# Optimization experiments

Measured on AMD Instinct MI355X. Metric: run time of the kernel, lower is better.

## Reference

```python
import jax, jax.numpy as jnp
import numpy as np

N, D_IN, Z, K = 65536, 512, 128, 1024


def setup_inputs() -> dict:
    key = jax.random.key(0)
    k1, k2, k3 = jax.random.split(key, 3)
    x = jax.random.normal(k1, (N, D_IN), dtype=jnp.float32)
    # Dense(z_units) params (glorot-ish scale)
    W = jax.random.normal(k2, (D_IN, Z), dtype=jnp.float32) * (1.0 / np.sqrt(D_IN))
    b = jnp.zeros((Z,), dtype=jnp.float32)
    # VQ codebook [k_discrete, z_units]
    codebook = jax.random.normal(k3, (K, Z), dtype=jnp.float32)
    return {"x": x, "W": W, "b": b, "codebook": codebook}


def reference(x, W, b, codebook):
    # z_embed: Dense projection to z_units
    z_continuous = x @ W + b  # [N, Z]
    # Euclidean distances to codebook entries, computed via the expanded
    # quadratic form (avoids materializing the [N, K, Z] broadcast tensor).
    sq = (jnp.sum(z_continuous * z_continuous, axis=-1, keepdims=True)
          - 2.0 * (z_continuous @ codebook.T)
          + jnp.sum(codebook * codebook, axis=-1))  # [N, K]
    distances = jnp.sqrt(jnp.maximum(sq, 0.0))
    k_nearest = jnp.argmin(distances, axis=-1)  # [N] int
    z_quantised = codebook[k_nearest]  # gather -> [N, Z]
    z_one_hot = jax.nn.one_hot(k_nearest, K, dtype=z_continuous.dtype)  # [N, K]
    # straight-through estimator
    z_straight_through = z_continuous + jax.lax.stop_gradient(z_quantised - z_continuous)
    # perplexity stats (stored as a layer attribute in the original; computed here
    # for faithfulness but not returned, matching call()'s return signature)
    avg_probs = jnp.mean(z_one_hot, axis=0)
    _perplexity = jnp.exp(-jnp.sum(avg_probs * jnp.log(avg_probs + 1e-10)))
    return (z_straight_through, z_quantised, z_continuous, z_one_hot)
```

## Files before the change

kernel.cpp:

```cpp
#include <hip/hip_runtime.h>
#include <cstddef>

#define NROWS 65536
#define DIN   512
#define ZDIM  128
#define KCB   1024

typedef float  f32x4  __attribute__((ext_vector_type(4)));
typedef short  short8 __attribute__((ext_vector_type(8)));
typedef __bf16 bf16x8 __attribute__((ext_vector_type(8)));
typedef unsigned short ushort_t;
typedef unsigned int   uint_t;

#define CB_CHB 24576
#define CB_SPB 8192
#define W_CHB  24576
#define W_SPB  8192
#define CNORM_OFF 786432
#define WF_OFF    790528
#define WS_NEEDED (790528 + 393216)

__device__ inline ushort_t bf_rtn(float v) {
  uint_t u = __float_as_uint(v);
  uint_t r = (u + 0x7fffu + ((u >> 16) & 1u)) >> 16;
  return (ushort_t)r;
}
__device__ inline float bf_up(ushort_t b) { return __uint_as_float(((uint_t)b) << 16); }
__device__ inline bf16x8 as_bf(short8 s) {
  union { short8 s; bf16x8 b; } u; u.s = s; return u.b;
}
__device__ inline void split3(float v, ushort_t& s1, ushort_t& s2, ushort_t& s3) {
  s1 = bf_rtn(v);  float f1 = bf_up(s1);
  float r1 = v - f1; s2 = bf_rtn(r1); float f2 = bf_up(s2);
  float r2 = r1 - f2; s3 = bf_rtn(r2);
}

__global__ __launch_bounds__(128) void ksplit2(
    const float* __restrict__ cbk, char* __restrict__ wsb)
{
  const int n = blockIdx.x, k = threadIdx.x;
  float v = cbk[(size_t)n * ZDIM + k];
  ushort_t s1, s2, s3; split3(v, s1, s2, s3);

  const int chunk = n >> 5, ct = (n >> 4) & 1;
  const int km = k & 31, ks = k >> 5;
  const int g = (km >> 2) & 3, h = (km >> 4) & 1, j = (km & 3) + 4 * h;
  const int l = 16 * g + (n & 15);
  char* base = wsb + chunk * CB_CHB + ct * 4096 + ks * 1024 + l * 16 + j * 2;
  *(ushort_t*)(base + 0 * CB_SPB) = s1;
  *(ushort_t*)(base + 1 * CB_SPB) = s2;
  *(ushort_t*)(base + 2 * CB_SPB) = s3;

  float c2 = v * v;
#pragma unroll
  for (int m = 1; m < 64; m <<= 1) c2 += __shfl_xor(c2, m);
  __shared__ float wsum[2];
  if ((threadIdx.x & 63) == 0) wsum[threadIdx.x >> 6] = c2;
  __syncthreads();
  if (threadIdx.x == 0)
    *(float*)(wsb + CNORM_OFF + (size_t)n * 4) = wsum[0] + wsum[1];
}

__global__ __launch_bounds__(256) void wsplit(
    const float* __restrict__ W, char* __restrict__ wsb)
{
  const int idx = blockIdx.x * 256 + threadIdx.x;
  const int k = idx >> 7, col = idx & 127;
  float v = W[(size_t)k * ZDIM + col];
  ushort_t s1, s2, s3; split3(v, s1, s2, s3);

  const int kc = k >> 5, km = k & 31;
  const int g = (km >> 2) & 3, h = (km >> 4) & 1, j = (km & 3) + 4 * h;
  const int ct = col >> 4, l = 16 * g + (col & 15);
  char* base = wsb + WF_OFF + kc * W_CHB + ct * 1024 + l * 16 + j * 2;
  *(ushort_t*)(base + 0 * W_SPB) = s1;
  *(ushort_t*)(base + 1 * W_SPB) = s2;
  *(ushort_t*)(base + 2 * W_SPB) = s3;
}

__global__ __launch_bounds__(256, 2) void k1_mfma(
    const float* __restrict__ x, const char* __restrict__ wfs,
    const float* __restrict__ b, float* __restrict__ z)
{
  __shared__ __align__(16) char wbuf[2 * W_CHB];

  const int t = threadIdx.x, w = t >> 6, l = t & 63;
  const int g = l >> 4, c16 = l & 15;
  const int bm = blockIdx.x;

  f32x4 acc[2][8];
#pragma unroll
  for (int rt = 0; rt < 2; ++rt)
#pragma unroll
    for (int ct = 0; ct < 8; ++ct) acc[rt][ct] = (f32x4){0.f, 0.f, 0.f, 0.f};

  const size_t rowb[2] = {
    ((size_t)bm * 128 + w * 32 + 0 * 16 + c16) * DIN,
    ((size_t)bm * 128 + w * 32 + 1 * 16 + c16) * DIN };

  f32x4 wreg[6];
#pragma unroll
  for (int it = 0; it < 6; ++it)
    wreg[it] = *(const f32x4*)(wfs + it * 4096 + t * 16);
  f32x4 xcur[2][2];
#pragma unroll
  for (int rt = 0; rt < 2; ++rt)
#pragma unroll
    for (int h = 0; h < 2; ++h)
      xcur[rt][h] = *(const f32x4*)(x + rowb[rt] + 4 * g + 16 * h);
#pragma unroll
  for (int it = 0; it < 6; ++it)
    *(f32x4*)(wbuf + it * 4096 + t * 16) = wreg[it];
  __syncthreads();

  for (int kc = 0; kc < 16; ++kc) {
    const char* buf = wbuf + (size_t)(kc & 1) * W_CHB;
    const bool more = (kc + 1) < 16;
    f32x4 xnext[2][2];
    if (more) {
#pragma unroll
      for (int it = 0; it < 6; ++it)
        wreg[it] = *(const f32x4*)(wfs + (size_t)(kc + 1) * W_CHB + it * 4096 + t * 16);
#pragma unroll
      for (int rt = 0; rt < 2; ++rt)
#pragma unroll
        for (int h = 0; h < 2; ++h)
          xnext[rt][h] = *(const f32x4*)(x + rowb[rt] + (kc + 1) * 32 + 4 * g + 16 * h);
    }

    short8 a1[2], a2[2], a3[2];
#pragma unroll
    for (int rt = 0; rt < 2; ++rt)
#pragma unroll
      for (int h = 0; h < 2; ++h)
#pragma unroll
        for (int j = 0; j < 4; ++j) {
          ushort_t q1, q2, q3; split3(xcur[rt][h][j], q1, q2, q3);
          a1[rt][4 * h + j] = (short)q1;
          a2[rt][4 * h + j] = (short)q2;
          a3[rt][4 * h + j] = (short)q3;
        }

#pragma unroll
    for (int ct = 0; ct < 8; ++ct) {
      const char* bp = buf + ct * 1024 + l * 16;
      short8 b1 = *(const short8*)(bp + 0 * W_SPB);
      short8 b2 = *(const short8*)(bp + 1 * W_SPB);
      short8 b3 = *(const short8*)(bp + 2 * W_SPB);
#pragma unroll
      for (int rt = 0; rt < 2; ++rt) {
        f32x4 a = acc[rt][ct];
        a = __builtin_amdgcn_mfma_f32_16x16x32_bf16(as_bf(a1[rt]), as_bf(b1), a, 0, 0, 0);
        a = __builtin_amdgcn_mfma_f32_16x16x32_bf16(as_bf(a1[rt]), as_bf(b2), a, 0, 0, 0);
        a = __builtin_amdgcn_mfma_f32_16x16x32_bf16(as_bf(a2[rt]), as_bf(b1), a, 0, 0, 0);
        a = __builtin_amdgcn_mfma_f32_16x16x32_bf16(as_bf(a1[rt]), as_bf(b3), a, 0, 0, 0);
        a = __builtin_amdgcn_mfma_f32_16x16x32_bf16(as_bf(a2[rt]), as_bf(b2), a, 0, 0, 0);
        a = __builtin_amdgcn_mfma_f32_16x16x32_bf16(as_bf(a3[rt]), as_bf(b1), a, 0, 0, 0);
        acc[rt][ct] = a;
      }
    }

    if (more) {
      char* nbuf = wbuf + (size_t)((kc + 1) & 1) * W_CHB;
#pragma unroll
      for (int it = 0; it < 6; ++it)
        *(f32x4*)(nbuf + it * 4096 + t * 16) = wreg[it];
#pragma unroll
      for (int rt = 0; rt < 2; ++rt)
#pragma unroll
        for (int h = 0; h < 2; ++h) xcur[rt][h] = xnext[rt][h];
    }
    __syncthreads();
  }

#pragma unroll
  for (int ct = 0; ct < 8; ++ct) {
    float bb = b[ct * 16 + c16];
#pragma unroll
    for (int rt = 0; rt < 2; ++rt)
#pragma unroll
      for (int i = 0; i < 4; ++i) {
        size_t row = (size_t)bm * 128 + w * 32 + rt * 16 + 4 * g + i;
        z[row * ZDIM + ct * 16 + c16] = acc[rt][ct][i] + bb;
      }
  }
}

__global__ __launch_bounds__(256, 2) void k2_mfma2(
    const float* __restrict__ zc, const float* __restrict__ cbk,
    const char* __restrict__ cbs, const float* __restrict__ cnorm,
    float* __restrict__ zst, float* __restrict__ zq, float* __restrict__ oh)
{
  __shared__ __align__(16) char buf2[2 * CB_CHB];
  __shared__ int karr[128];

  const int t = threadIdx.x, w = t >> 6, l = t & 63;
  const int g = l >> 4, c16 = l & 15;
  const int bm = blockIdx.x;

  f32x4 streg[6];
#pragma unroll
  for (int it = 0; it < 6; ++it)
    streg[it] = *(const f32x4*)(cbs + it * 4096 + t * 16);

  short8 a1[2][4], a2[2][4], a3[2][4];
  float anorm[2][4];
#pragma unroll
  for (int rt = 0; rt < 2; ++rt) {
    const size_t rb = ((size_t)bm * 128 + w * 32 + rt * 16 + c16) * ZDIM;
    float psum = 0.f;
#pragma unroll
    for (int ks = 0; ks < 4; ++ks)
#pragma unroll
      for (int h = 0; h < 2; ++h) {
        f32x4 v = *(const f32x4*)(zc + rb + ks * 32 + 4 * g + 16 * h);
#pragma unroll
        for (int j = 0; j < 4; ++j) {
          ushort_t q1, q2, q3; split3(v[j], q1, q2, q3);
          a1[rt][ks][4 * h + j] = (short)q1;
          a2[rt][ks][4 * h + j] = (short)q2;
          a3[rt][ks][4 * h + j] = (short)q3;
          psum += v[j] * v[j];
        }
      }
    psum += __shfl_xor(psum, 16);
    psum += __shfl_xor(psum, 32);
#pragma unroll
    for (int i = 0; i < 4; ++i) anorm[rt][i] = __shfl(psum, 4 * g + i);
  }

#pragma unroll
  for (int it = 0; it < 6; ++it)
    *(f32x4*)(buf2 + it * 4096 + t * 16) = streg[it];
  __syncthreads();

  float fmin[2][4]; int kmin[2][4];
#pragma unroll
  for (int rt = 0; rt < 2; ++rt)
#pragma unroll
    for (int i = 0; i < 4; ++i) { fmin[rt][i] = 3.402823466e38f; kmin[rt][i] = 0; }

  for (int c = 0; c < 32; ++c) {
    const char* buf = buf2 + (size_t)(c & 1) * CB_CHB;
    const bool more = (c + 1) < 32;
    if (more) {
#pragma unroll
      for (int it = 0; it < 6; ++it)
        streg[it] = *(const f32x4*)(cbs + (size_t)(c + 1) * CB_CHB + it * 4096 + t * 16);
    }

    {
      const size_t orow = (size_t)(bm * 128 + c * 4 + (t >> 6)) * KCB;
#pragma unroll
      for (int u = 0; u < 4; ++u) {
        f32x4 zv = {0.f, 0.f, 0.f, 0.f};
        *(f32x4*)(oh + orow + (t & 63) * 4 + u * 256) = zv;
      }
    }

    float cn0 = cnorm[c * 32 + c16];
    float cn1 = cnorm[c * 32 + 16 + c16];

#pragma unroll
    for (int ct = 0; ct < 2; ++ct) {
      f32x4 pa[2];
#pragma unroll
      for (int rt = 0; rt < 2; ++rt) pa[rt] = (f32x4){0.f, 0.f, 0.f, 0.f};
#pragma unroll
      for (int ks = 0; ks < 4; ++ks) {
        const char* bp = buf + ct * 4096 + ks * 1024 + l * 16;
        short8 b1 = *(const short8*)(bp + 0 * CB_SPB);
        short8 b2 = *(const short8*)(bp + 1 * CB_SPB);
        short8 b3 = *(const short8*)(bp + 2 * CB_SPB);
#pragma unroll
        for (int rt = 0; rt < 2; ++rt) {
          f32x4 a = pa[rt];
          a = __builtin_amdgcn_mfma_f32_16x16x32_bf16(as_bf(a1[rt][ks]), as_bf(b1), a, 0, 0, 0);
          a = __builtin_amdgcn_mfma_f32_16x16x32_bf16(as_bf(a1[rt][ks]), as_bf(b2), a, 0, 0, 0);
          a = __builtin_amdgcn_mfma_f32_16x16x32_bf16(as_bf(a2[rt][ks]), as_bf(b1), a, 0, 0, 0);
          a = __builtin_amdgcn_mfma_f32_16x16x32_bf16(as_bf(a1[rt][ks]), as_bf(b3), a, 0, 0, 0);
          a = __builtin_amdgcn_mfma_f32_16x16x32_bf16(as_bf(a2[rt][ks]), as_bf(b2), a, 0, 0, 0);
          a = __builtin_amdgcn_mfma_f32_16x16x32_bf16(as_bf(a3[rt][ks]), as_bf(b1), a, 0, 0, 0);
          pa[rt] = a;
        }
      }
      const int colb = c * 32 + ct * 16 + c16;
      const float cn = ct ? cn1 : cn0;
#pragma unroll
      for (int rt = 0; rt < 2; ++rt)
#pragma unroll
        for (int i = 0; i < 4; ++i) {
          float f = (anorm[rt][i] - 2.f * pa[rt][i]) + cn;
          if (f < fmin[rt][i]) { fmin[rt][i] = f; kmin[rt][i] = colb; }
        }
    }

    if (more) {
      char* nbuf = buf2 + (size_t)((c + 1) & 1) * CB_CHB;
#pragma unroll
      for (int it = 0; it < 6; ++it)
        *(f32x4*)(nbuf + it * 4096 + t * 16) = streg[it];
    }
    __syncthreads();
  }

#pragma unroll
  for (int m = 1; m < 16; m <<= 1) {
#pragma unroll
    for (int rt = 0; rt < 2; ++rt)
#pragma unroll
      for (int i = 0; i < 4; ++i) {
        float f2 = __shfl_xor(fmin[rt][i], m);
        int   k2 = __shfl_xor(kmin[rt][i], m);
        if (f2 < fmin[rt][i] || (f2 == fmin[rt][i] && k2 < kmin[rt][i])) {
          fmin[rt][i] = f2; kmin[rt][i] = k2;
        }
      }
  }
  if (c16 == 0) {
#pragma unroll
    for (int rt = 0; rt < 2; ++rt)
#pragma unroll
      for (int i = 0; i < 4; ++i)
        karr[w * 32 + rt * 16 + 4 * g + i] = kmin[rt][i];
  }
  __syncthreads();

  for (int it = 0; it < 64; ++it) {
    int r = it * 2 + (t >> 7);
    int col = t & 127;
    size_t row = (size_t)bm * 128 + r;
    float v = cbk[(size_t)karr[r] * ZDIM + col];
    zst[row * ZDIM + col] = v;
    zq[row * ZDIM + col] = v;
  }

  if (t < 128) {
    oh[(size_t)(bm * 128 + t) * KCB + karr[t]] = 1.0f;
  }
}

__global__ __launch_bounds__(256) void k1_gemm(
    const float* __restrict__ x, const float* __restrict__ W,
    const float* __restrict__ b, float* __restrict__ z)
{
  __shared__ float xs[32][68];
  __shared__ float ws[32][132];

  const int t  = threadIdx.x;
  const int tx = t & 15, ty = t >> 4;
  const int bm = blockIdx.x;

  float acc[4][8];
#pragma unroll
  for (int i = 0; i < 4; ++i)
#pragma unroll
    for (int j = 0; j < 8; ++j) acc[i][j] = 0.f;

  const int sr  = t >> 2;
  const int skb = (t & 3) * 8;
  const int wkk = t >> 3;
  const int wcol = (t & 7) * 16;

  for (int k0 = 0; k0 < DIN; k0 += 32) {
    float4 v0 = *reinterpret_cast<const float4*>(&x[(size_t)(bm * 64 + sr) * DIN + k0 + skb]);
    float4 v1 = *reinterpret_cast<const float4*>(&x[(size_t)(bm * 64 + sr) * DIN + k0 + skb + 4]);
    xs[skb + 0][sr] = v0.x; xs[skb + 1][sr] = v0.y; xs[skb + 2][sr] = v0.z; xs[skb + 3][sr] = v0.w;
    xs[skb + 4][sr] = v1.x; xs[skb + 5][sr] = v1.y; xs[skb + 6][sr] = v1.z; xs[skb + 7][sr] = v1.w;
#pragma unroll
    for (int u = 0; u < 4; ++u) {
      float4 wv = *reinterpret_cast<const float4*>(&W[(size_t)(k0 + wkk) * ZDIM + wcol + u * 4]);
      *reinterpret_cast<float4*>(&ws[wkk][wcol + u * 4]) = wv;
    }
    __syncthreads();
#pragma unroll
    for (int kk = 0; kk < 32; ++kk) {
      float4 xv = *reinterpret_cast<float4*>(&xs[kk][ty * 4]);
      float4 wa = *reinterpret_cast<float4*>(&ws[kk][tx * 4]);
      float4 wb = *reinterpret_cast<float4*>(&ws[kk][64 + tx * 4]);
      float xr[4] = {xv.x, xv.y, xv.z, xv.w};
      float wr[8] = {wa.x, wa.y, wa.z, wa.w, wb.x, wb.y, wb.z, wb.w};
#pragma unroll
      for (int i = 0; i < 4; ++i)
#pragma unroll
        for (int j = 0; j < 8; ++j) acc[i][j] += xr[i] * wr[j];
    }
    __syncthreads();
  }

  float4 ba = *reinterpret_cast<const float4*>(&b[tx * 4]);
  float4 bb = *reinterpret_cast<const float4*>(&b[64 + tx * 4]);
#pragma unroll
  for (int i = 0; i < 4; ++i) {
    size_t row = (size_t)bm * 64 + ty * 4 + i;
    float4 oa = {acc[i][0] + ba.x, acc[i][1] + ba.y, acc[i][2] + ba.z, acc[i][3] + ba.w};
    float4 ob = {acc[i][4] + bb.x, acc[i][5] + bb.y, acc[i][6] + bb.z, acc[i][7] + bb.w};
    *reinterpret_cast<float4*>(&z[row * ZDIM + tx * 4]) = oa;
    *reinterpret_cast<float4*>(&z[row * ZDIM + 64 + tx * 4]) = ob;
  }
}

__global__ __launch_bounds__(256) void k2_vq(
    const float* __restrict__ zc, const float* __restrict__ cbk,
    float* __restrict__ zst, float* __restrict__ zq, float* __restrict__ oh)
{
  __shared__ float zt[128][68];
  __shared__ float ct[32][132];
  __shared__ float pc[128][2];
  __shared__ float csqc[128];
  __shared__ float Ap[64][4];
  __shared__ float Al[64];
  __shared__ float fbuf[64][17];
  __shared__ int   ibuf[64][17];
  __shared__ int   karr[64];

  const int t  = threadIdx.x;
  const int tx = t & 15, ty = t >> 4;
  const int bm = blockIdx.x;

  {
    const int r = t >> 2, kb = (t & 3) * 32;
    float asum = 0.f;
#pragma unroll
    for (int u = 0; u < 8; ++u) {
      float4 v = *reinterpret_cast<const float4*>(&zc[(size_t)(bm * 64 + r) * ZDIM + kb + u * 4]);
      zt[kb + u * 4 + 0][r] = v.x; zt[kb + u * 4 + 1][r] = v.y;
      zt[kb + u * 4 + 2][r] = v.z; zt[kb + u * 4 + 3][r] = v.w;
      asum += v.x * v.x + v.y * v.y + v.z * v.z + v.w * v.w;
    }
    Ap[r][t & 3] = asum;
  }
  __syncthreads();
  if (t < 64) Al[t] = (Ap[t][0] + Ap[t][1]) + (Ap[t][2] + Ap[t][3]);

  float fmin[4];
  int   kmin[4];
#pragma unroll
  for (int i = 0; i < 4; ++i) { fmin[i] = 3.4e38f; kmin[i] = 0; }

  const int scol = t >> 1, skb = (t & 1) * 16;

  for (int chunk = 0; chunk < 8; ++chunk) {
    float acc[4][8];
#pragma unroll
    for (int i = 0; i < 4; ++i)
#pragma unroll
      for (int j = 0; j < 8; ++j) acc[i][j] = 0.f;
    float cpart = 0.f;

    for (int ks = 0; ks < 4; ++ks) {
      __syncthreads();
#pragma unroll
      for (int u = 0; u < 4; ++u) {
        float4 v = *reinterpret_cast<const float4*>(
            &cbk[(size_t)(chunk * 128 + scol) * ZDIM + ks * 32 + skb + u * 4]);
        ct[skb + u * 4 + 0][scol] = v.x; ct[skb + u * 4 + 1][scol] = v.y;
        ct[skb + u * 4 + 2][scol] = v.z; ct[skb + u * 4 + 3][scol] = v.w;
        cpart += v.x * v.x + v.y * v.y + v.z * v.z + v.w * v.w;
      }
      __syncthreads();
#pragma unroll
      for (int kk = 0; kk < 32; ++kk) {
        float4 xv = *reinterpret_cast<float4*>(&zt[ks * 32 + kk][ty * 4]);
        float4 wa = *reinterpret_cast<float4*>(&ct[kk][tx * 4]);
        float4 wb = *reinterpret_cast<float4*>(&ct[kk][64 + tx * 4]);
        float xr[4] = {xv.x, xv.y, xv.z, xv.w};
        float wr[8] = {wa.x, wa.y, wa.z, wa.w, wb.x, wb.y, wb.z, wb.w};
#pragma unroll
        for (int i = 0; i < 4; ++i)
#pragma unroll
          for (int j = 0; j < 8; ++j) acc[i][j] += xr[i] * wr[j];
      }
    }

    pc[scol][t & 1] = cpart;
    __syncthreads();
    if (t < 128) csqc[t] = pc[t][0] + pc[t][1];
    __syncthreads();

#pragma unroll
    for (int i = 0; i < 4; ++i) {
      float Ar = Al[ty * 4 + i];
#pragma unroll
      for (int j = 0; j < 8; ++j) {
        int colL = (j < 4) ? (tx * 4 + j) : (64 + tx * 4 + (j - 4));
        float B = 2.f * acc[i][j];
        float f = (Ar - B) + csqc[colL];
        int col = chunk * 128 + colL;
        if (f < fmin[i] || (f == fmin[i] && col < kmin[i])) { fmin[i] = f; kmin[i] = col; }
      }
    }
  }

#pragma unroll
  for (int i = 0; i < 4; ++i) { fbuf[ty * 4 + i][tx] = fmin[i]; ibuf[ty * 4 + i][tx] = kmin[i]; }
  __syncthreads();
  if (t < 64) {
    float bf = fbuf[t][0]; int bi = ibuf[t][0];
    for (int e = 1; e < 16; ++e) {
      float f2 = fbuf[t][e]; int i2 = ibuf[t][e];
      if (f2 < bf || (f2 == bf && i2 < bi)) { bf = f2; bi = i2; }
    }
    karr[t] = bi;
  }
  __syncthreads();

  for (int it = 0; it < 32; ++it) {
    int r = it * 2 + (t >> 7);
    int col = t & 127;
    size_t row = (size_t)bm * 64 + r;
    float v = cbk[(size_t)karr[r] * ZDIM + col];
    zst[row * ZDIM + col] = v;
    zq[row * ZDIM + col] = v;
  }

  for (int r = 0; r < 64; ++r) {
    int k = karr[r];
    float4 v = {0.f, 0.f, 0.f, 0.f};
    if ((k >> 2) == t) {
      float* vv = reinterpret_cast<float*>(&v);
      vv[k & 3] = 1.f;
    }
    *reinterpret_cast<float4*>(&oh[(size_t)(bm * 64 + r) * KCB + t * 4]) = v;
  }
}

extern "C" void kernel_launch(void* const* d_in, const int* in_sizes, int n_in,
                              void* d_out, int out_size, void* d_ws, size_t ws_size,
                              hipStream_t stream) {
  const float* x   = (const float*)d_in[0];
  const float* W   = (const float*)d_in[1];
  const float* b   = (const float*)d_in[2];
  const float* cbk = (const float*)d_in[3];

  float* out = (float*)d_out;
  float* zst = out;
  float* zq  = out + (size_t)NROWS * ZDIM;
  float* zc  = out + (size_t)2 * NROWS * ZDIM;
  float* oh  = out + (size_t)3 * NROWS * ZDIM;

  if (ws_size >= (size_t)WS_NEEDED) {
    char* wsb = (char*)d_ws;
    ksplit2<<<KCB, 128, 0, stream>>>(cbk, wsb);
    wsplit<<<256, 256, 0, stream>>>(W, wsb);
    k1_mfma<<<NROWS / 128, 256, 0, stream>>>(x, wsb + WF_OFF, b, zc);
    k2_mfma2<<<NROWS / 128, 256, 0, stream>>>(
        zc, cbk, wsb, (const float*)(wsb + CNORM_OFF), zst, zq, oh);
  } else {
    k1_gemm<<<NROWS / 64, 256, 0, stream>>>(x, W, b, zc);
    k2_vq<<<NROWS / 64, 256, 0, stream>>>(zc, cbk, zst, zq, oh);
  }
}
```

Before: 169.0 us.

## Fuse projection GEMM and VQ distance kernel, staging z tile in LDS

Merges the projection kernel and the codebook-distance kernel into one launch. Each block keeps its 128x128 z tile in a swizzled shared-memory buffer, so the VQ stage no longer reads z back from global memory. The kernel also prefetches codebook norms one chunk ahead, uses nontemporal stores for the zc, one-hot, zq and zst outputs, and vectorises the gather of codebook rows. In exchange, shared memory per block grows to 64KB plus karr, which may limit occupancy to fewer blocks per CU than the launch bound of 2 requests.

```diff
diff --git a/kernel.cpp b/kernel.cpp
--- a/kernel.cpp
+++ b/kernel.cpp
@@ -19,6 +19,8 @@
 #define CNORM_OFF 786432
 #define WF_OFF    790528
 #define WS_NEEDED (790528 + 393216)
+
+#define ZWORD(r, c) ((r) * 128 + ((c) ^ (((r) & 7) << 2)))
 
 __device__ inline ushort_t bf_rtn(float v) {
   uint_t u = __float_as_uint(v);
@@ -78,11 +80,16 @@
   *(ushort_t*)(base + 2 * W_SPB) = s3;
 }
 
-__global__ __launch_bounds__(256, 2) void k1_mfma(
+__global__ __launch_bounds__(256, 2) void fused(
     const float* __restrict__ x, const char* __restrict__ wfs,
-    const float* __restrict__ b, float* __restrict__ z)
+    const float* __restrict__ b, const char* __restrict__ cbs,
+    const float* __restrict__ cnorm, const float* __restrict__ cbk,
+    float* __restrict__ zst, float* __restrict__ zq,
+    float* __restrict__ zc, float* __restrict__ oh)
 {
-  __shared__ __align__(16) char wbuf[2 * W_CHB];
+  __shared__ __align__(16) char smem[65536];
+  __shared__ int karr[128];
+  float* zw = (float*)smem;
 
   const int t = threadIdx.x, w = t >> 6, l = t & 63;
   const int g = l >> 4, c16 = l & 15;
@@ -110,11 +117,11 @@
       xcur[rt][h] = *(const f32x4*)(x + rowb[rt] + 4 * g + 16 * h);
 #pragma unroll
   for (int it = 0; it < 6; ++it)
-    *(f32x4*)(wbuf + it * 4096 + t * 16) = wreg[it];
+    *(f32x4*)(smem + it * 4096 + t * 16) = wreg[it];
   __syncthreads();
 
   for (int kc = 0; kc < 16; ++kc) {
-    const char* buf = wbuf + (size_t)(kc & 1) * W_CHB;
+    const char* buf = smem + (size_t)(kc & 1) * W_CHB;
     const bool more = (kc + 1) < 16;
     f32x4 xnext[2][2];
     if (more) {
@@ -161,7 +168,7 @@
     }
 
     if (more) {
-      char* nbuf = wbuf + (size_t)((kc + 1) & 1) * W_CHB;
+      char* nbuf = smem + (size_t)((kc + 1) & 1) * W_CHB;
 #pragma unroll
       for (int it = 0; it < 6; ++it)
         *(f32x4*)(nbuf + it * 4096 + t * 16) = wreg[it];
@@ -176,50 +183,40 @@
 #pragma unroll
   for (int ct = 0; ct < 8; ++ct) {
     float bb = b[ct * 16 + c16];
+    const int col = ct * 16 + c16;
 #pragma unroll
     for (int rt = 0; rt < 2; ++rt)
 #pragma unroll
       for (int i = 0; i < 4; ++i) {
-        size_t row = (size_t)bm * 128 + w * 32 + rt * 16 + 4 * g + i;
-        z[row * ZDIM + ct * 16 + c16] = acc[rt][ct][i] + bb;
-      }
-  }
-}
-
-__global__ __launch_bounds__(256, 2) void k2_mfma2(
-    const float* __restrict__ zc, const float* __restrict__ cbk,
-    const char* __restrict__ cbs, const float* __restrict__ cnorm,
-    float* __restrict__ zst, float* __restrict__ zq, float* __restrict__ oh)
-{
-  __shared__ __align__(16) char buf2[2 * CB_CHB];
-  __shared__ int karr[128];
-
-  const int t = threadIdx.x, w = t >> 6, l = t & 63;
-  const int g = l >> 4, c16 = l & 15;
-  const int bm = blockIdx.x;
+        const int rl = w * 32 + rt * 16 + 4 * g + i;
+        zw[ZWORD(rl, col)] = acc[rt][ct][i] + bb;
+      }
+  }
+  __syncthreads();
 
   f32x4 streg[6];
 #pragma unroll
   for (int it = 0; it < 6; ++it)
     streg[it] = *(const f32x4*)(cbs + it * 4096 + t * 16);
 
-  short8 a1[2][4], a2[2][4], a3[2][4];
+  short8 a1f[2][4], a2f[2][4], a3f[2][4];
   float anorm[2][4];
 #pragma unroll
   for (int rt = 0; rt < 2; ++rt) {
-    const size_t rb = ((size_t)bm * 128 + w * 32 + rt * 16 + c16) * ZDIM;
+    const int rl = w * 32 + rt * 16 + c16;
     float psum = 0.f;
 #pragma unroll
     for (int ks = 0; ks < 4; ++ks)
 #pragma unroll
       for (int h = 0; h < 2; ++h) {
-        f32x4 v = *(const f32x4*)(zc + rb + ks * 32 + 4 * g + 16 * h);
+        const int c0 = ks * 32 + 4 * g + 16 * h;
+        f32x4 v = *(const f32x4*)&zw[ZWORD(rl, c0)];
 #pragma unroll
         for (int j = 0; j < 4; ++j) {
           ushort_t q1, q2, q3; split3(v[j], q1, q2, q3);
-          a1[rt][ks][4 * h + j] = (short)q1;
-          a2[rt][ks][4 * h + j] = (short)q2;
-          a3[rt][ks][4 * h + j] = (short)q3;
+          a1f[rt][ks][4 * h + j] = (short)q1;
+          a2f[rt][ks][4 * h + j] = (short)q2;
+          a3f[rt][ks][4 * h + j] = (short)q3;
           psum += v[j] * v[j];
         }
       }
@@ -229,9 +226,20 @@
     for (int i = 0; i < 4; ++i) anorm[rt][i] = __shfl(psum, 4 * g + i);
   }
 
+  {
+    const int r = t >> 1, half = (t & 1) * 64;
+    float* dst = zc + ((size_t)bm * 128 + r) * ZDIM;
+#pragma unroll
+    for (int u = 0; u < 16; ++u) {
+      const int c0 = half + u * 4;
+      f32x4 v = *(const f32x4*)&zw[ZWORD(r, c0)];
+      __builtin_nontemporal_store(v, (f32x4*)(dst + c0));
+    }
+  }
+  __syncthreads();
 #pragma unroll
   for (int it = 0; it < 6; ++it)
-    *(f32x4*)(buf2 + it * 4096 + t * 16) = streg[it];
+    *(f32x4*)(smem + it * 4096 + t * 16) = streg[it];
   __syncthreads();
 
   float fmin[2][4]; int kmin[2][4];
@@ -240,26 +248,27 @@
 #pragma unroll
     for (int i = 0; i < 4; ++i) { fmin[rt][i] = 3.402823466e38f; kmin[rt][i] = 0; }
 
+  float cn0 = cnorm[c16], cn1 = cnorm[16 + c16];
+
   for (int c = 0; c < 32; ++c) {
-    const char* buf = buf2 + (size_t)(c & 1) * CB_CHB;
+    const char* buf = smem + (size_t)(c & 1) * CB_CHB;
     const bool more = (c + 1) < 32;
+    float cn0n = 0.f, cn1n = 0.f;
     if (more) {
 #pragma unroll
       for (int it = 0; it < 6; ++it)
         streg[it] = *(const f32x4*)(cbs + (size_t)(c + 1) * CB_CHB + it * 4096 + t * 16);
+      cn0n = cnorm[(c + 1) * 32 + c16];
+      cn1n = cnorm[(c + 1) * 32 + 16 + c16];
     }
 
     {
-      const size_t orow = (size_t)(bm * 128 + c * 4 + (t >> 6)) * KCB;
-#pragma unroll
-      for (int u = 0; u < 4; ++u) {
-        f32x4 zv = {0.f, 0.f, 0.f, 0.f};
-        *(f32x4*)(oh + orow + (t & 63) * 4 + u * 256) = zv;
-      }
-    }
-
-    float cn0 = cnorm[c * 32 + c16];
-    float cn1 = cnorm[c * 32 + 16 + c16];
+      float* orow = oh + (size_t)(bm * 128 + c * 4 + (t >> 6)) * KCB + (t & 63) * 4;
+      const f32x4 zv = {0.f, 0.f, 0.f, 0.f};
+#pragma unroll
+      for (int u = 0; u < 4; ++u)
+        __builtin_nontemporal_store(zv, (f32x4*)(orow + u * 256));
+    }
 
 #pragma unroll
     for (int ct = 0; ct < 2; ++ct) {
@@ -275,12 +284,12 @@
 #pragma unroll
         for (int rt = 0; rt < 2; ++rt) {
           f32x4 a = pa[rt];
-          a = __builtin_amdgcn_mfma_f32_16x16x32_bf16(as_bf(a1[rt][ks]), as_bf(b1), a, 0, 0, 0);
-          a = __builtin_amdgcn_mfma_f32_16x16x32_bf16(as_bf(a1[rt][ks]), as_bf(b2), a, 0, 0, 0);
-          a = __builtin_amdgcn_mfma_f32_16x16x32_bf16(as_bf(a2[rt][ks]), as_bf(b1), a, 0, 0, 0);
-          a = __builtin_amdgcn_mfma_f32_16x16x32_bf16(as_bf(a1[rt][ks]), as_bf(b3), a, 0, 0, 0);
-          a = __builtin_amdgcn_mfma_f32_16x16x32_bf16(as_bf(a2[rt][ks]), as_bf(b2), a, 0, 0, 0);
-          a = __builtin_amdgcn_mfma_f32_16x16x32_bf16(as_bf(a3[rt][ks]), as_bf(b1), a, 0, 0, 0);
+          a = __builtin_amdgcn_mfma_f32_16x16x32_bf16(as_bf(a1f[rt][ks]), as_bf(b1), a, 0, 0, 0);
+          a = __builtin_amdgcn_mfma_f32_16x16x32_bf16(as_bf(a1f[rt][ks]), as_bf(b2), a, 0, 0, 0);
+          a = __builtin_amdgcn_mfma_f32_16x16x32_bf16(as_bf(a2f[rt][ks]), as_bf(b1), a, 0, 0, 0);
+          a = __builtin_amdgcn_mfma_f32_16x16x32_bf16(as_bf(a1f[rt][ks]), as_bf(b3), a, 0, 0, 0);
+          a = __builtin_amdgcn_mfma_f32_16x16x32_bf16(as_bf(a2f[rt][ks]), as_bf(b2), a, 0, 0, 0);
+          a = __builtin_amdgcn_mfma_f32_16x16x32_bf16(as_bf(a3f[rt][ks]), as_bf(b1), a, 0, 0, 0);
           pa[rt] = a;
         }
       }
@@ -296,10 +305,11 @@
     }
 
     if (more) {
-      char* nbuf = buf2 + (size_t)((c + 1) & 1) * CB_CHB;
+      char* nbuf = smem + (size_t)((c + 1) & 1) * CB_CHB;
 #pragma unroll
       for (int it = 0; it < 6; ++it)
         *(f32x4*)(nbuf + it * 4096 + t * 16) = streg[it];
+      cn0 = cn0n; cn1 = cn1n;
     }
     __syncthreads();
   }
@@ -326,13 +336,14 @@
   }
   __syncthreads();
 
-  for (int it = 0; it < 64; ++it) {
-    int r = it * 2 + (t >> 7);
-    int col = t & 127;
-    size_t row = (size_t)bm * 128 + r;
-    float v = cbk[(size_t)karr[r] * ZDIM + col];
-    zst[row * ZDIM + col] = v;
-    zq[row * ZDIM + col] = v;
+#pragma unroll
+  for (int it = 0; it < 16; ++it) {
+    const int idx = it * 256 + t;
+    const int r = idx >> 5, cq = (idx & 31) * 4;
+    f32x4 v = *(const f32x4*)&cbk[(size_t)karr[r] * ZDIM + cq];
+    const size_t off = ((size_t)bm * 128 + r) * ZDIM + cq;
+    __builtin_nontemporal_store(v, (f32x4*)(zst + off));
+    __builtin_nontemporal_store(v, (f32x4*)(zq + off));
   }
 
   if (t < 128) {
@@ -543,9 +554,9 @@
     char* wsb = (char*)d_ws;
     ksplit2<<<KCB, 128, 0, stream>>>(cbk, wsb);
     wsplit<<<256, 256, 0, stream>>>(W, wsb);
-    k1_mfma<<<NROWS / 128, 256, 0, stream>>>(x, wsb + WF_OFF, b, zc);
-    k2_mfma2<<<NROWS / 128, 256, 0, stream>>>(
-        zc, cbk, wsb, (const float*)(wsb + CNORM_OFF), zst, zq, oh);
+    fused<<<NROWS / 128, 256, 0, stream>>>(
+        x, wsb + WF_OFF, b, wsb, (const float*)(wsb + CNORM_OFF), cbk,
+        zst, zq, zc, oh);
   } else {
     k1_gemm<<<NROWS / 64, 256, 0, stream>>>(x, W, b, zc);
     k2_vq<<<NROWS / 64, 256, 0, stream>>>(zc, cbk, zst, zq, oh);
```

Result: slower. 212.9 us (+26.0%).

## Use single-bf16 distance pass with candidate threshold and exact fp32 refinement

Applied to the files above, without the earlier changes.

The distance GEMM now uses a single bf16 MFMA term instead of six split-precision products. It makes two passes: one to find an approximate per-row minimum, and one to collect codes within a margin of it, which are then rescored exactly in fp32 and reduced through atomic 64-bit keys. Zeroing the one-hot output moves into the projection kernel with nontemporal stores, and the gather writes become vectorized. Risks: the 0.25*sqrt(|z|^2) margin is a heuristic that might miss the true argmin, and the codebook is now streamed twice.

```diff
diff --git a/kernel.cpp b/kernel.cpp
--- a/kernel.cpp
+++ b/kernel.cpp
@@ -11,6 +11,7 @@
 typedef __bf16 bf16x8 __attribute__((ext_vector_type(8)));
 typedef unsigned short ushort_t;
 typedef unsigned int   uint_t;
+typedef unsigned long long u64_t;
 
 #define CB_CHB 24576
 #define CB_SPB 8192
@@ -33,6 +34,37 @@
   s1 = bf_rtn(v);  float f1 = bf_up(s1);
   float r1 = v - f1; s2 = bf_rtn(r1); float f2 = bf_up(s2);
   float r2 = r1 - f2; s3 = bf_rtn(r2);
+}
+
+__device__ inline void refine_one(uint_t packed, int bm, int w,
+    const float* __restrict__ zc, const float* __restrict__ cbk,
+    const float* __restrict__ cnorm, u64_t* rowkey)
+{
+  const int col = packed & 1023;
+  const int rowloc = (packed >> 10) & 31;
+  const int r = w * 32 + rowloc;
+  const float* zr = zc + ((size_t)bm * 128 + r) * ZDIM;
+  const float* cr = cbk + (size_t)col * ZDIM;
+  f32x4 dps = {0.f, 0.f, 0.f, 0.f}, aps = {0.f, 0.f, 0.f, 0.f};
+#pragma unroll
+  for (int u = 0; u < 32; ++u) {
+    f32x4 zv = *(const f32x4*)(zr + u * 4);
+    f32x4 cv = *(const f32x4*)(cr + u * 4);
+    dps += zv * cv;
+    aps += zv * zv;
+  }
+  float dot = (dps[0] + dps[1]) + (dps[2] + dps[3]);
+  float A   = (aps[0] + aps[1]) + (aps[2] + aps[3]);
+  float d = (A - 2.f * dot) + cnorm[col];
+  uint_t db = __float_as_uint(d);
+  db = (db & 0x80000000u) ? ~db : (db | 0x80000000u);
+  u64_t key = ((u64_t)db << 32) | (uint_t)col;
+  u64_t old = rowkey[r];
+  while (key < old) {
+    u64_t assumed = old;
+    old = atomicCAS(&rowkey[r], assumed, key);
+    if (old == assumed) break;
+  }
 }
 
 __global__ __launch_bounds__(128) void ksplit2(
@@ -78,9 +110,10 @@
   *(ushort_t*)(base + 2 * W_SPB) = s3;
 }
 
-__global__ __launch_bounds__(256, 2) void k1_mfma(
+__global__ __launch_bounds__(256, 2) void k1_oh(
     const float* __restrict__ x, const char* __restrict__ wfs,
-    const float* __restrict__ b, float* __restrict__ z)
+    const float* __restrict__ b, float* __restrict__ z,
+    float* __restrict__ oh)
 {
   __shared__ __align__(16) char wbuf[2 * W_CHB];
 
@@ -126,6 +159,14 @@
 #pragma unroll
         for (int h = 0; h < 2; ++h)
           xnext[rt][h] = *(const f32x4*)(x + rowb[rt] + (kc + 1) * 32 + 4 * g + 16 * h);
+    }
+
+    {
+      float* orow = oh + ((size_t)bm * 128 + kc * 8 + (t >> 5)) * KCB + (t & 31) * 4;
+      const f32x4 zv4 = {0.f, 0.f, 0.f, 0.f};
+#pragma unroll
+      for (int u = 0; u < 8; ++u)
+        __builtin_nontemporal_store(zv4, (f32x4*)(orow + u * 128));
     }
 
     short8 a1[2], a2[2], a3[2];
@@ -186,24 +227,25 @@
   }
 }
 
-__global__ __launch_bounds__(256, 2) void k2_mfma2(
+__global__ __launch_bounds__(256, 2) void k2f(
     const float* __restrict__ zc, const float* __restrict__ cbk,
     const char* __restrict__ cbs, const float* __restrict__ cnorm,
     float* __restrict__ zst, float* __restrict__ zq, float* __restrict__ oh)
 {
-  __shared__ __align__(16) char buf2[2 * CB_CHB];
+  __shared__ __align__(16) char sm[16384];
+  __shared__ u64_t rowkey[128];
+  __shared__ uint_t wpool[4][128];
+  __shared__ int wcnt[4];
   __shared__ int karr[128];
 
   const int t = threadIdx.x, w = t >> 6, l = t & 63;
   const int g = l >> 4, c16 = l & 15;
   const int bm = blockIdx.x;
 
-  f32x4 streg[6];
-#pragma unroll
-  for (int it = 0; it < 6; ++it)
-    streg[it] = *(const f32x4*)(cbs + it * 4096 + t * 16);
-
-  short8 a1[2][4], a2[2][4], a3[2][4];
+  if (t < 128) rowkey[t] = ~0ull;
+  if (t < 4) wcnt[t] = 0;
+
+  short8 a1f[2][4];
   float anorm[2][4];
 #pragma unroll
   for (int rt = 0; rt < 2; ++rt) {
@@ -216,10 +258,7 @@
         f32x4 v = *(const f32x4*)(zc + rb + ks * 32 + 4 * g + 16 * h);
 #pragma unroll
         for (int j = 0; j < 4; ++j) {
-          ushort_t q1, q2, q3; split3(v[j], q1, q2, q3);
-          a1[rt][ks][4 * h + j] = (short)q1;
-          a2[rt][ks][4 * h + j] = (short)q2;
-          a3[rt][ks][4 * h + j] = (short)q3;
+          a1f[rt][ks][4 * h + j] = (short)bf_rtn(v[j]);
           psum += v[j] * v[j];
         }
       }
@@ -229,37 +268,31 @@
     for (int i = 0; i < 4; ++i) anorm[rt][i] = __shfl(psum, 4 * g + i);
   }
 
-#pragma unroll
-  for (int it = 0; it < 6; ++it)
-    *(f32x4*)(buf2 + it * 4096 + t * 16) = streg[it];
-  __syncthreads();
-
-  float fmin[2][4]; int kmin[2][4];
+  float m1[2][4];
 #pragma unroll
   for (int rt = 0; rt < 2; ++rt)
 #pragma unroll
-    for (int i = 0; i < 4; ++i) { fmin[rt][i] = 3.402823466e38f; kmin[rt][i] = 0; }
+    for (int i = 0; i < 4; ++i) m1[rt][i] = 3.402823466e38f;
+
+  f32x4 streg[2];
+#pragma unroll
+  for (int it = 0; it < 2; ++it)
+    streg[it] = *(const f32x4*)(cbs + it * 4096 + t * 16);
+#pragma unroll
+  for (int it = 0; it < 2; ++it)
+    *(f32x4*)(sm + it * 4096 + t * 16) = streg[it];
+  __syncthreads();
 
   for (int c = 0; c < 32; ++c) {
-    const char* buf = buf2 + (size_t)(c & 1) * CB_CHB;
+    const char* buf = sm + (size_t)(c & 1) * 8192;
     const bool more = (c + 1) < 32;
     if (more) {
 #pragma unroll
-      for (int it = 0; it < 6; ++it)
+      for (int it = 0; it < 2; ++it)
         streg[it] = *(const f32x4*)(cbs + (size_t)(c + 1) * CB_CHB + it * 4096 + t * 16);
     }
-
-    {
-      const size_t orow = (size_t)(bm * 128 + c * 4 + (t >> 6)) * KCB;
-#pragma unroll
-      for (int u = 0; u < 4; ++u) {
-        f32x4 zv = {0.f, 0.f, 0.f, 0.f};
-        *(f32x4*)(oh + orow + (t & 63) * 4 + u * 256) = zv;
-      }
-    }
-
-    float cn0 = cnorm[c * 32 + c16];
-    float cn1 = cnorm[c * 32 + 16 + c16];
+    const float cn0 = cnorm[c * 32 + c16];
+    const float cn1 = cnorm[c * 32 + 16 + c16];
 
 #pragma unroll
     for (int ct = 0; ct < 2; ++ct) {
@@ -268,71 +301,116 @@
       for (int rt = 0; rt < 2; ++rt) pa[rt] = (f32x4){0.f, 0.f, 0.f, 0.f};
 #pragma unroll
       for (int ks = 0; ks < 4; ++ks) {
-        const char* bp = buf + ct * 4096 + ks * 1024 + l * 16;
-        short8 b1 = *(const short8*)(bp + 0 * CB_SPB);
-        short8 b2 = *(const short8*)(bp + 1 * CB_SPB);
-        short8 b3 = *(const short8*)(bp + 2 * CB_SPB);
-#pragma unroll
-        for (int rt = 0; rt < 2; ++rt) {
-          f32x4 a = pa[rt];
-          a = __builtin_amdgcn_mfma_f32_16x16x32_bf16(as_bf(a1[rt][ks]), as_bf(b1), a, 0, 0, 0);
-          a = __builtin_amdgcn_mfma_f32_16x16x32_bf16(as_bf(a1[rt][ks]), as_bf(b2), a, 0, 0, 0);
-          a = __builtin_amdgcn_mfma_f32_16x16x32_bf16(as_bf(a2[rt][ks]), as_bf(b1), a, 0, 0, 0);
-          a = __builtin_amdgcn_mfma_f32_16x16x32_bf16(as_bf(a1[rt][ks]), as_bf(b3), a, 0, 0, 0);
-          a = __builtin_amdgcn_mfma_f32_16x16x32_bf16(as_bf(a2[rt][ks]), as_bf(b2), a, 0, 0, 0);
-          a = __builtin_amdgcn_mfma_f32_16x16x32_bf16(as_bf(a3[rt][ks]), as_bf(b1), a, 0, 0, 0);
-          pa[rt] = a;
-        }
-      }
-      const int colb = c * 32 + ct * 16 + c16;
+        short8 b1 = *(const short8*)(buf + ct * 4096 + ks * 1024 + l * 16);
+#pragma unroll
+        for (int rt = 0; rt < 2; ++rt)
+          pa[rt] = __builtin_amdgcn_mfma_f32_16x16x32_bf16(as_bf(a1f[rt][ks]), as_bf(b1), pa[rt], 0, 0, 0);
+      }
       const float cn = ct ? cn1 : cn0;
 #pragma unroll
       for (int rt = 0; rt < 2; ++rt)
 #pragma unroll
         for (int i = 0; i < 4; ++i) {
           float f = (anorm[rt][i] - 2.f * pa[rt][i]) + cn;
-          if (f < fmin[rt][i]) { fmin[rt][i] = f; kmin[rt][i] = colb; }
+          m1[rt][i] = fminf(m1[rt][i], f);
         }
     }
 
     if (more) {
-      char* nbuf = buf2 + (size_t)((c + 1) & 1) * CB_CHB;
-#pragma unroll
-      for (int it = 0; it < 6; ++it)
+      char* nbuf = sm + (size_t)((c + 1) & 1) * 8192;
+#pragma unroll
+      for (int it = 0; it < 2; ++it)
         *(f32x4*)(nbuf + it * 4096 + t * 16) = streg[it];
     }
     __syncthreads();
   }
 
 #pragma unroll
-  for (int m = 1; m < 16; m <<= 1) {
+  for (int m = 1; m < 16; m <<= 1)
 #pragma unroll
     for (int rt = 0; rt < 2; ++rt)
 #pragma unroll
-      for (int i = 0; i < 4; ++i) {
-        float f2 = __shfl_xor(fmin[rt][i], m);
-        int   k2 = __shfl_xor(kmin[rt][i], m);
-        if (f2 < fmin[rt][i] || (f2 == fmin[rt][i] && k2 < kmin[rt][i])) {
-          fmin[rt][i] = f2; kmin[rt][i] = k2;
+      for (int i = 0; i < 4; ++i)
+        m1[rt][i] = fminf(m1[rt][i], __shfl_xor(m1[rt][i], m));
+
+  float thr[2][4];
+#pragma unroll
+  for (int rt = 0; rt < 2; ++rt)
+#pragma unroll
+    for (int i = 0; i < 4; ++i)
+      thr[rt][i] = m1[rt][i] + 0.25f * sqrtf(anorm[rt][i]);
+
+#pragma unroll
+  for (int it = 0; it < 2; ++it)
+    streg[it] = *(const f32x4*)(cbs + it * 4096 + t * 16);
+#pragma unroll
+  for (int it = 0; it < 2; ++it)
+    *(f32x4*)(sm + it * 4096 + t * 16) = streg[it];
+  __syncthreads();
+
+  for (int c = 0; c < 32; ++c) {
+    const char* buf = sm + (size_t)(c & 1) * 8192;
+    const bool more = (c + 1) < 32;
+    if (more) {
+#pragma unroll
+      for (int it = 0; it < 2; ++it)
+        streg[it] = *(const f32x4*)(cbs + (size_t)(c + 1) * CB_CHB + it * 4096 + t * 16);
+    }
+    const float cn0 = cnorm[c * 32 + c16];
+    const float cn1 = cnorm[c * 32 + 16 + c16];
+
+#pragma unroll
+    for (int ct = 0; ct < 2; ++ct) {
+      f32x4 pa[2];
+#pragma unroll
+      for (int rt = 0; rt < 2; ++rt) pa[rt] = (f32x4){0.f, 0.f, 0.f, 0.f};
+#pragma unroll
+      for (int ks = 0; ks < 4; ++ks) {
+        short8 b1 = *(const short8*)(buf + ct * 4096 + ks * 1024 + l * 16);
+#pragma unroll
+        for (int rt = 0; rt < 2; ++rt)
+          pa[rt] = __builtin_amdgcn_mfma_f32_16x16x32_bf16(as_bf(a1f[rt][ks]), as_bf(b1), pa[rt], 0, 0, 0);
+      }
+      const float cn = ct ? cn1 : cn0;
+      const int colb = c * 32 + ct * 16 + c16;
+#pragma unroll
+      for (int rt = 0; rt < 2; ++rt)
+#pragma unroll
+        for (int i = 0; i < 4; ++i) {
+          float f = (anorm[rt][i] - 2.f * pa[rt][i]) + cn;
+          if (f <= thr[rt][i]) {
+            uint_t packed = (uint_t)colb | ((uint_t)(rt * 16 + 4 * g + i) << 10);
+            int slot = atomicAdd(&wcnt[w], 1);
+            if (slot < 128) wpool[w][slot] = packed;
+            else refine_one(packed, bm, w, zc, cbk, cnorm, rowkey);
+          }
         }
-      }
-  }
-  if (c16 == 0) {
-#pragma unroll
-    for (int rt = 0; rt < 2; ++rt)
-#pragma unroll
-      for (int i = 0; i < 4; ++i)
-        karr[w * 32 + rt * 16 + 4 * g + i] = kmin[rt][i];
-  }
-  __syncthreads();
-
-  for (int it = 0; it < 64; ++it) {
-    int r = it * 2 + (t >> 7);
-    int col = t & 127;
-    size_t row = (size_t)bm * 128 + r;
-    float v = cbk[(size_t)karr[r] * ZDIM + col];
-    zst[row * ZDIM + col] = v;
-    zq[row * ZDIM + col] = v;
+    }
+
+    if (more) {
+      char* nbuf = sm + (size_t)((c + 1) & 1) * 8192;
+#pragma unroll
+      for (int it = 0; it < 2; ++it)
+        *(f32x4*)(nbuf + it * 4096 + t * 16) = streg[it];
+    }
+    __syncthreads();
+  }
+
+  int cnt = wcnt[w]; if (cnt > 128) cnt = 128;
+  for (int s = l; s < cnt; s += 64)
+    refine_one(wpool[w][s], bm, w, zc, cbk, cnorm, rowkey);
+  __syncthreads();
+  if (t < 128) karr[t] = (int)(rowkey[t] & 1023ull);
+  __syncthreads();
+
+#pragma unroll
+  for (int it = 0; it < 16; ++it) {
+    const int idx = it * 256 + t;
+    const int r = idx >> 5, cq = (idx & 31) * 4;
+    f32x4 v = *(const f32x4*)&cbk[(size_t)karr[r] * ZDIM + cq];
+    const size_t off = ((size_t)bm * 128 + r) * ZDIM + cq;
+    __builtin_nontemporal_store(v, (f32x4*)(zst + off));
+    __builtin_nontemporal_store(v, (f32x4*)(zq + off));
   }
 
   if (t < 128) {
@@ -543,8 +621,8 @@
     char* wsb = (char*)d_ws;
     ksplit2<<<KCB, 128, 0, stream>>>(cbk, wsb);
     wsplit<<<256, 256, 0, stream>>>(W, wsb);
-    k1_mfma<<<NROWS / 128, 256, 0, stream>>>(x, wsb + WF_OFF, b, zc);
-    k2_mfma2<<<NROWS / 128, 256, 0, stream>>>(
+    k1_oh<<<NROWS / 128, 256, 0, stream>>>(x, wsb + WF_OFF, b, zc, oh);
+    k2f<<<NROWS / 128, 256, 0, stream>>>(
         zc, cbk, wsb, (const float*)(wsb + CNORM_OFF), zst, zq, oh);
   } else {
     k1_gemm<<<NROWS / 64, 256, 0, stream>>>(x, W, b, zc);
```

New measurement: 150.5 us. -10.9%, faster.
